# Performance work log

Measured on AMD Instinct MI355X. Metric: run time of the kernel, lower is better.

The kernel has to match this reference:

```python
import jax, jax.numpy as jnp
import numpy as np

DIN = 1024
DOUT = 1024

def setup_inputs() -> dict:
    key = jax.random.key(0)
    kx, kq, kk, kv = jax.random.split(key, 4)
    x = jax.random.normal(kx, (4, 2048, DIN), dtype=jnp.float32)
    s = 1.0 / np.sqrt(DIN)
    Wq = jax.random.uniform(kq, (DIN, DOUT), dtype=jnp.float32, minval=-s, maxval=s)
    Wk = jax.random.uniform(kk, (DIN, DOUT), dtype=jnp.float32, minval=-s, maxval=s)
    Wv = jax.random.uniform(kv, (DIN, DOUT), dtype=jnp.float32, minval=-s, maxval=s)
    return {"x": x, "Wq": Wq, "Wk": Wk, "Wv": Wv}

def reference(x, Wq, Wk, Wv):
    # q,k,v: [B, T, D]
    q = jnp.einsum('btd,de->bte', x, Wq)
    k = jnp.einsum('btd,de->bte', x, Wk)
    v = jnp.einsum('btd,de->bte', x, Wv)
    # scores: [B, T_q, T_k]; NOTE: no 1/sqrt(d) scaling in original
    scores = jnp.einsum('bqd,bkd->bqk', q, k)
    # Original applies softmax over dim=1 (the QUERY axis), faithfully kept
    weights = jax.nn.softmax(scores, axis=1)
    return jnp.einsum('bqk,bkd->bqd', weights, v)
```

## Files before the change

kernel.cpp:

```cpp
#include <hip/hip_runtime.h>

#define B_   4
#define T_   2048
#define D_   1024
#define MTOK 8192

typedef __attribute__((ext_vector_type(8))) _Float16 half8;
typedef __attribute__((ext_vector_type(4))) float    f32x4;

#define GLD(G, L) __builtin_amdgcn_global_load_lds(                       \
    (const __attribute__((address_space(1))) void*)(G),                   \
    (__attribute__((address_space(3))) void*)(L), 16, 0, 0)

#define BAR()   __builtin_amdgcn_s_barrier()
#define BARM()  asm volatile("s_barrier" ::: "memory")
#define LGKM0() do { asm volatile("s_waitcnt lgkmcnt(0)" ::: "memory");   \
                     __builtin_amdgcn_sched_barrier(0); } while (0)
#define VMW3()  asm volatile("s_waitcnt vmcnt(3)" ::: "memory")
#define VMW1()  asm volatile("s_waitcnt vmcnt(1)" ::: "memory")
#define VMW0()  asm volatile("s_waitcnt vmcnt(0)" ::: "memory")

__device__ __forceinline__ unsigned short f2h(float f) {
  return __builtin_bit_cast(unsigned short, (_Float16)f);
}
__device__ __forceinline__ float h2f(unsigned short u) {
  return (float)__builtin_bit_cast(_Float16, u);
}

__global__ __launch_bounds__(256) void tofp16_kernel(
    const float4* __restrict__ in, ushort4* __restrict__ out, int n4,
    float4* __restrict__ cs, int c4) {
  int i = blockIdx.x * 256 + threadIdx.x;
  if (i < c4) cs[i] = (float4){0.f, 0.f, 0.f, 0.f};
  if (i >= n4) return;
  float4 v = in[i];
  ushort4 h;
  h.x = f2h(v.x); h.y = f2h(v.y); h.z = f2h(v.z); h.w = f2h(v.w);
  out[i] = h;
}

__global__ __launch_bounds__(256) void wcat_t_kernel(
    const float* __restrict__ Wq, const float* __restrict__ Wk,
    const float* __restrict__ Wv, unsigned short* __restrict__ Wt) {
  __shared__ float tile[32][33];
  int z = blockIdx.z;
  const float* W = (z == 0) ? Wq : ((z == 1) ? Wk : Wv);
  int c0 = blockIdx.x * 32, r0 = blockIdx.y * 32;
  int tx = threadIdx.x & 31, ty = threadIdx.x >> 5;
  #pragma unroll
  for (int i = 0; i < 4; ++i)
    tile[ty + i * 8][tx] = W[(size_t)(r0 + ty + i * 8) * D_ + c0 + tx];
  __syncthreads();
  #pragma unroll
  for (int i = 0; i < 4; ++i) {
    float v = tile[tx][ty + i * 8];
    size_t row = (size_t)z * D_ + c0 + ty + i * 8;
    Wt[row * D_ + r0 + tx] = f2h(v);
  }
}

__global__ __launch_bounds__(256) void vtrans_kernel(
    const unsigned short* __restrict__ QKV, unsigned short* __restrict__ Vt) {
  __shared__ unsigned short tile[64][68];
  int b = blockIdx.z;
  int t0 = blockIdx.x * 64, d0 = blockIdx.y * 64;
  int l16 = threadIdx.x & 15, rr = threadIdx.x >> 4;
  const unsigned short* src =
      QKV + ((size_t)b * 2048 + t0 + rr) * 3072 + 2048 + d0 + l16 * 4;
  #pragma unroll
  for (int i = 0; i < 4; ++i) {
    ushort4 v = *(const ushort4*)(src + (size_t)i * 16 * 3072);
    *(ushort4*)&tile[rr + i * 16][l16 * 4] = v;
  }
  __syncthreads();
  unsigned short* dst = Vt + ((size_t)b * D_ + d0) * 2048 + t0;
  #pragma unroll
  for (int j = 0; j < 4; ++j) {
    int dd = rr + j * 16;
    int tt = l16 * 4;
    ushort4 v;
    v.x = tile[tt + 0][dd]; v.y = tile[tt + 1][dd];
    v.z = tile[tt + 2][dd]; v.w = tile[tt + 3][dd];
    *(ushort4*)(dst + (size_t)dd * 2048 + tt) = v;
  }
}

template <int EPI>
__global__ __launch_bounds__(512, 4) void gemm8p(
    const unsigned short* __restrict__ A, const unsigned short* __restrict__ B,
    void* __restrict__ C0, float* __restrict__ CS,
    int K, int lda, int ldb, int ldc,
    long aBatch, long bBatch, long cBatch) {
  constexpr int ABY  = 128 * 64;
  constexpr int BUFB = ABY + 16384;
  __shared__ __align__(16) char lds[2 * BUFB];

  const int z = blockIdx.z;
  A += (size_t)z * aBatch;
  B += (size_t)z * bBatch;

  const int nwg = gridDim.x * gridDim.y;
  int s = blockIdx.y * gridDim.x + blockIdx.x;
  s = (s & 7) * (nwg >> 3) + (s >> 3);
  const int bx = s % gridDim.x, by = s / gridDim.x;
  const int brow = by * 128, bcol = bx * 256;

  const int tid = threadIdx.x;
  const int wid = tid >> 6, lane = tid & 63;
  const int wr = wid >> 2, wc = wid & 3;
  const int l15 = lane & 15, g4 = lane >> 4;

  const int scol = ((lane & 3) ^ ((lane >> 3) & 3)) * 8;
  const int srow = lane >> 2;
  int aoff, adst, boffs[2], bdst[2];
  {
    int r0 = wid * 16;
    aoff = (brow + r0 + srow) * lda + scol;
    adst = r0 * 64;
    #pragma unroll
    for (int rg = 0; rg < 2; ++rg) {
      int rb = (wid >> 1) * 64 + rg * 32 + (wid & 1) * 16;
      boffs[rg] = (bcol + rb + srow) * ldb + scol;
      bdst[rg]  = ABY + rb * 64;
    }
  }

  const int rslot = (g4 ^ ((l15 >> 1) & 3)) * 16;
  int aRd[2], bRd[2];
  #pragma unroll
  for (int mh = 0; mh < 2; ++mh) {
    aRd[mh] = (wr * 64 + mh * 32 + l15) * 64 + rslot;
    bRd[mh] = ABY + (wc * 64 + mh * 32 + l15) * 64 + rslot;
  }

#define STAGE_A(bb, tt) \
    GLD(A + (size_t)(aoff + (tt) * 32), lds + (bb) * BUFB + adst)
#define STAGE_B(nh, bb, tt) \
    GLD(B + (size_t)(boffs[nh] + (tt) * 32), lds + (bb) * BUFB + bdst[nh])
#define LOAD_A(mh) do { _Pragma("unroll")                                     \
    for (int mf = 0; mf < 2; ++mf)                                            \
      ar[mf] = *(const half8*)(buf + aRd[mh] + mf * 1024); } while (0)
#define LOAD_B(dst, nh) do { _Pragma("unroll")                                \
    for (int nf = 0; nf < 2; ++nf)                                            \
      dst[nf] = *(const half8*)(buf + bRd[nh] + nf * 1024); } while (0)
#define MFMA_Q(mh, nh, br) do { _Pragma("unroll")                             \
    for (int mf = 0; mf < 2; ++mf) { _Pragma("unroll")                        \
      for (int nf = 0; nf < 2; ++nf) {                                        \
        f32x4& ac = acc[(mh) * 2 + mf][(nh) * 2 + nf];                        \
        ac = __builtin_amdgcn_mfma_f32_16x16x32_f16(ar[mf], br[nf], ac, 0, 0, 0); \
      } } } while (0)

  STAGE_A(0, 0); STAGE_B(0, 0, 0); STAGE_B(1, 0, 0);
  STAGE_A(1, 1); STAGE_B(0, 1, 1); STAGE_B(1, 1, 1);
  VMW3();
  BAR();

  f32x4 acc[4][4] = {};
  half8 ar[2], b0r[2], b1r[2];
  const int nIter = K / 64;

  for (int it = 0; it < nIter; ++it) {
    const bool st = (it + 1 < nIter);
    #pragma unroll
    for (int h = 0; h < 2; ++h) {
      const char* buf = lds + h * BUFB;
      const int tt = 2 * it + 2 + h;
      LOAD_A(0); LOAD_B(b0r, 0);
      BAR(); LGKM0();
      __builtin_amdgcn_s_setprio(1); MFMA_Q(0, 0, b0r);
      __builtin_amdgcn_s_setprio(0); BAR();
      LOAD_B(b1r, 1);
      if (st) STAGE_B(0, h, tt);
      BAR(); LGKM0();
      __builtin_amdgcn_s_setprio(1); MFMA_Q(0, 1, b1r);
      __builtin_amdgcn_s_setprio(0); BAR();
      LOAD_A(1);
      if (st) STAGE_B(1, h, tt);
      BAR(); LGKM0();
      __builtin_amdgcn_s_setprio(1); MFMA_Q(1, 1, b1r);
      __builtin_amdgcn_s_setprio(0); BAR();
      if (st) STAGE_A(h, tt);
      BAR();
      __builtin_amdgcn_s_setprio(1); MFMA_Q(1, 0, b0r);
      __builtin_amdgcn_s_setprio(0);
      if (st) { VMW3(); } else { VMW0(); }
      BAR();
    }
  }

  if constexpr (EPI == 1) {
    unsigned short* C = (unsigned short*)C0 + (size_t)z * cBatch;
    #pragma unroll
    for (int m = 0; m < 4; ++m) {
      int rowoff = (m >> 1) * 32 + (m & 1) * 16;
      #pragma unroll
      for (int n = 0; n < 4; ++n) {
        int coloff = (n >> 1) * 32 + (n & 1) * 16;
        #pragma unroll
        for (int r = 0; r < 4; ++r) {
          int row = brow + wr * 64 + rowoff + g4 * 4 + r;
          int col = bcol + wc * 64 + coloff + l15;
          C[(size_t)row * ldc + col] = f2h(acc[m][n][r]);
        }
      }
    }
  } else {
    unsigned short* C = (unsigned short*)C0 + (size_t)z * cBatch;
    float csum[4] = {0.f, 0.f, 0.f, 0.f};
    #pragma unroll
    for (int m = 0; m < 4; ++m) {
      int rowoff = (m >> 1) * 32 + (m & 1) * 16;
      #pragma unroll
      for (int n = 0; n < 4; ++n) {
        int coloff = (n >> 1) * 32 + (n & 1) * 16;
        #pragma unroll
        for (int r = 0; r < 4; ++r) {
          int row = brow + wr * 64 + rowoff + g4 * 4 + r;
          int col = bcol + wc * 64 + coloff + l15;
          unsigned short hh = f2h(acc[m][n][r]);
          C[(size_t)row * ldc + col] = hh;
          csum[n] += __expf(h2f(hh) - 64.0f);
        }
      }
    }
    #pragma unroll
    for (int n = 0; n < 4; ++n) {
      csum[n] += __shfl_xor(csum[n], 16);
      csum[n] += __shfl_xor(csum[n], 32);
    }
    if (g4 == 0) {
      #pragma unroll
      for (int n = 0; n < 4; ++n) {
        int col = bcol + wc * 64 + (n >> 1) * 32 + (n & 1) * 16 + l15;
        unsafeAtomicAdd(CS + (size_t)z * T_ + col, csum[n]);
      }
    }
  }
#undef STAGE_A
#undef STAGE_B
#undef LOAD_A
#undef LOAD_B
#undef MFMA_Q
}

__global__ __launch_bounds__(512, 4) void gemmPV(
    const unsigned short* __restrict__ Sc, const float* __restrict__ U,
    const unsigned short* __restrict__ Bv, float* __restrict__ out) {
  constexpr int ABY  = 128 * 64;
  constexpr int BUFB = ABY + 8192;
  __shared__ __align__(16) char lds[3 * BUFB];

  const int b = blockIdx.z;
  Sc += (size_t)b * T_ * T_;
  U  += (size_t)b * T_;
  Bv += (size_t)b * D_ * T_;
  float* Co = out + (size_t)b * T_ * D_;

  const int nwg = gridDim.x * gridDim.y;
  int s = blockIdx.y * gridDim.x + blockIdx.x;
  s = (s & 7) * (nwg >> 3) + (s >> 3);
  const int bx = s % gridDim.x, by = s / gridDim.x;
  const int brow = by * 128, bcol = bx * 128;

  const int tid = threadIdx.x;
  const int wid = tid >> 6, lane = tid & 63;
  const int wr = wid >> 2, wc = wid & 3;
  const int l15 = lane & 15, g4 = lane >> 4;

  const int arow = wid * 16 + (lane >> 2);
  const unsigned short* aSrc = Sc + (size_t)(brow + arow) * T_ + (lane & 3) * 8;
  const int awB  = arow * 64 + ((lane & 3) ^ ((lane >> 3) & 3)) * 16;
  const int ucol = (lane & 3) * 8;

  const int scol = ((lane & 3) ^ ((lane >> 3) & 3)) * 8;
  const int boff = (bcol + wid * 16 + (lane >> 2)) * T_ + scol;
  const int bdst = ABY + wid * 1024;

  const int rslot = (g4 ^ ((l15 >> 1) & 3)) * 16;
  int aRd[4], bRd[2];
  #pragma unroll
  for (int mf = 0; mf < 4; ++mf)
    aRd[mf] = (wr * 64 + mf * 16 + l15) * 64 + rslot;
  #pragma unroll
  for (int nf = 0; nf < 2; ++nf)
    bRd[nf] = ABY + (wc * 32 + nf * 16 + l15) * 64 + rslot;

  uint4 rawA;
  float4 uva, uvb;

#define PV_AISSUE(tt) do {                                                    \
    rawA = *(const uint4*)(aSrc + (size_t)(tt) * 32);                         \
    uva  = *(const float4*)(U + (tt) * 32 + ucol);                            \
    uvb  = *(const float4*)(U + (tt) * 32 + ucol + 4); } while (0)
#define PV_AWRITE(base) do {                                                  \
    const unsigned short* hp = (const unsigned short*)&rawA;                  \
    float uu[8] = {uva.x, uva.y, uva.z, uva.w, uvb.x, uvb.y, uvb.z, uvb.w};   \
    unsigned int w_[4];                                                       \
    _Pragma("unroll") for (int j = 0; j < 4; ++j) {                           \
      float w0 = __expf(h2f(hp[2 * j])     - 64.f) * uu[2 * j];               \
      float w1 = __expf(h2f(hp[2 * j + 1]) - 64.f) * uu[2 * j + 1];           \
      w_[j] = (unsigned int)f2h(w0) | ((unsigned int)f2h(w1) << 16); }        \
    *(uint4*)((base) + awB) = *(uint4*)w_; } while (0)

  char* bufA = lds;
  char* bufB = lds + BUFB;
  char* bufC = lds + 2 * BUFB;

  PV_AISSUE(0);
  GLD(Bv + (size_t)(boff + 0), bufA + bdst);
  uint4  rawA1 = *(const uint4*)(aSrc + 32);
  float4 uva1  = *(const float4*)(U + 32 + ucol);
  float4 uvb1  = *(const float4*)(U + 32 + ucol + 4);
  GLD(Bv + (size_t)(boff + 32), bufB + bdst);
  VMW1();
  PV_AWRITE(bufA);
  rawA = rawA1; uva = uva1; uvb = uvb1;
  PV_AWRITE(bufB);
  asm volatile("s_waitcnt lgkmcnt(0)" ::: "memory");

  f32x4 acc[4][2] = {};
  half8 ar[4], br[2];
  const int NT = T_ / 32;

  for (int t = 0; t < NT; ++t) {
    BARM();
    const bool st = (t + 2 < NT);
    if (st) {
      PV_AISSUE(t + 2);
      GLD(Bv + (size_t)(boff + (t + 2) * 32), bufC + bdst);
    }
    #pragma unroll
    for (int mf = 0; mf < 4; ++mf)
      ar[mf] = *(const half8*)(bufA + aRd[mf]);
    #pragma unroll
    for (int nf = 0; nf < 2; ++nf)
      br[nf] = *(const half8*)(bufA + bRd[nf]);
    __builtin_amdgcn_s_setprio(1);
    #pragma unroll
    for (int mf = 0; mf < 4; ++mf)
      #pragma unroll
      for (int nf = 0; nf < 2; ++nf)
        acc[mf][nf] = __builtin_amdgcn_mfma_f32_16x16x32_f16(ar[mf], br[nf], acc[mf][nf], 0, 0, 0);
    __builtin_amdgcn_s_setprio(0);
    if (st) {
      VMW1();
      PV_AWRITE(bufC);
      asm volatile("s_waitcnt lgkmcnt(0)" ::: "memory");
    } else if (t + 2 == NT) {
      VMW0();
    }
    char* tmp = bufA; bufA = bufB; bufB = bufC; bufC = tmp;
  }

  #pragma unroll
  for (int mf = 0; mf < 4; ++mf)
    #pragma unroll
    for (int nf = 0; nf < 2; ++nf)
      #pragma unroll
      for (int r = 0; r < 4; ++r) {
        int row = brow + wr * 64 + mf * 16 + g4 * 4 + r;
        int col = bcol + wc * 32 + nf * 16 + l15;
        Co[(size_t)row * D_ + col] = acc[mf][nf][r];
      }
#undef PV_AISSUE
#undef PV_AWRITE
}

__global__ __launch_bounds__(256) void sm_stats(const float* __restrict__ cs,
                                                float* __restrict__ stats) {
  int i = blockIdx.x * 256 + threadIdx.x;
  stats[i] = 1.0f / cs[i];
}

extern "C" void kernel_launch(void* const* d_in, const int* in_sizes, int n_in,
                              void* d_out, int out_size, void* d_ws, size_t ws_size,
                              hipStream_t stream) {
  const float* x  = (const float*)d_in[0];
  const float* Wq = (const float*)d_in[1];
  const float* Wk = (const float*)d_in[2];
  const float* Wv = (const float*)d_in[3];
  float* out = (float*)d_out;

  char* ws = (char*)d_ws;
  const size_t MB = 1024ull * 1024ull;
  unsigned short* scoresh = (unsigned short*)(ws);
  unsigned short* QKVh = (unsigned short*)(ws + 32 * MB);
  unsigned short* Vt   = (unsigned short*)(ws + 80 * MB);
  unsigned short* xh   = (unsigned short*)(ws + 96 * MB);
  unsigned short* Wt   = (unsigned short*)(ws + 112 * MB);
  float* colsum = (float*)(ws + 118 * MB);
  float* stats  = (float*)(ws + 118 * MB + 64 * 1024);

  tofp16_kernel<<<MTOK * D_ / 4 / 256, 256, 0, stream>>>(
      (const float4*)x, (ushort4*)xh, MTOK * D_ / 4,
      (float4*)colsum, B_ * T_ / 4);

  wcat_t_kernel<<<dim3(32, 32, 3), 256, 0, stream>>>(Wq, Wk, Wv, Wt);

  gemm8p<1><<<dim3(3072 / 256, MTOK / 128, 1), 512, 0, stream>>>(
      xh, Wt, QKVh, nullptr, D_, D_, D_, 3072, 0, 0, 0);

  vtrans_kernel<<<dim3(T_ / 64, D_ / 64, B_), 256, 0, stream>>>(QKVh, Vt);

  gemm8p<2><<<dim3(T_ / 256, T_ / 128, B_), 512, 0, stream>>>(
      QKVh, QKVh + 1024, scoresh, colsum, D_, 3072, 3072, T_,
      (long)T_ * 3072, (long)T_ * 3072, (long)T_ * T_);

  sm_stats<<<B_ * T_ / 256, 256, 0, stream>>>(colsum, stats);

  gemmPV<<<dim3(D_ / 128, T_ / 128, B_), 512, 0, stream>>>(
      scoresh, stats, Vt, out);
}
```

Before: 201.5 us.

## Retile PV GEMM to 64x256 blocks with 4 waves, 64x64 per wave

Reshapes the PV GEMM tile from 128x128 with 8 waves to 64x256 with 4 waves, so each wave computes a 64x64 output block. Each wave reuses A fragments across more B columns, and the exp/scale transform of scores is done for only 64 rows per block, which cuts redundant exp work per output element. The cost is higher register pressure from doubling the accumulators, fewer waves per block, a larger B staging buffer, and changed vmcnt wait counts.

```diff
diff --git a/kernel.cpp b/kernel.cpp
--- a/kernel.cpp
+++ b/kernel.cpp
@@ -16,9 +16,7 @@
 #define BARM()  asm volatile("s_barrier" ::: "memory")
 #define LGKM0() do { asm volatile("s_waitcnt lgkmcnt(0)" ::: "memory");   \
                      __builtin_amdgcn_sched_barrier(0); } while (0)
-#define VMW3()  asm volatile("s_waitcnt vmcnt(3)" ::: "memory")
-#define VMW1()  asm volatile("s_waitcnt vmcnt(1)" ::: "memory")
-#define VMW0()  asm volatile("s_waitcnt vmcnt(0)" ::: "memory")
+#define VMW(n)  asm volatile("s_waitcnt vmcnt(" #n ")" ::: "memory")
 
 __device__ __forceinline__ unsigned short f2h(float f) {
   return __builtin_bit_cast(unsigned short, (_Float16)f);
@@ -152,7 +150,7 @@
 
   STAGE_A(0, 0); STAGE_B(0, 0, 0); STAGE_B(1, 0, 0);
   STAGE_A(1, 1); STAGE_B(0, 1, 1); STAGE_B(1, 1, 1);
-  VMW3();
+  VMW(3);
   BAR();
 
   f32x4 acc[4][4] = {};
@@ -183,7 +181,7 @@
       BAR();
       __builtin_amdgcn_s_setprio(1); MFMA_Q(1, 0, b0r);
       __builtin_amdgcn_s_setprio(0);
-      if (st) { VMW3(); } else { VMW0(); }
+      if (st) { VMW(3); } else { VMW(0); }
       BAR();
     }
   }
@@ -243,11 +241,11 @@
 #undef MFMA_Q
 }
 
-__global__ __launch_bounds__(512, 4) void gemmPV(
+__global__ __launch_bounds__(256, 2) void gemmPV(
     const unsigned short* __restrict__ Sc, const float* __restrict__ U,
     const unsigned short* __restrict__ Bv, float* __restrict__ out) {
-  constexpr int ABY  = 128 * 64;
-  constexpr int BUFB = ABY + 8192;
+  constexpr int ABY  = 64 * 64;
+  constexpr int BUFB = ABY + 16384;
   __shared__ __align__(16) char lds[3 * BUFB];
 
   const int b = blockIdx.z;
@@ -260,34 +258,42 @@
   int s = blockIdx.y * gridDim.x + blockIdx.x;
   s = (s & 7) * (nwg >> 3) + (s >> 3);
   const int bx = s % gridDim.x, by = s / gridDim.x;
-  const int brow = by * 128, bcol = bx * 128;
+  const int brow = by * 64, bcol = bx * 256;
 
   const int tid = threadIdx.x;
   const int wid = tid >> 6, lane = tid & 63;
-  const int wr = wid >> 2, wc = wid & 3;
   const int l15 = lane & 15, g4 = lane >> 4;
 
-  const int arow = wid * 16 + (lane >> 2);
-  const unsigned short* aSrc = Sc + (size_t)(brow + arow) * T_ + (lane & 3) * 8;
-  const int awB  = arow * 64 + ((lane & 3) ^ ((lane >> 3) & 3)) * 16;
-  const int ucol = (lane & 3) * 8;
+  const int arow = tid >> 2;
+  const unsigned short* aSrc = Sc + (size_t)(brow + arow) * T_ + (tid & 3) * 8;
+  const int awB  = arow * 64 + ((tid & 3) ^ ((tid >> 3) & 3)) * 16;
+  const int ucol = (tid & 3) * 8;
 
   const int scol = ((lane & 3) ^ ((lane >> 3) & 3)) * 8;
-  const int boff = (bcol + wid * 16 + (lane >> 2)) * T_ + scol;
-  const int bdst = ABY + wid * 1024;
+  const int srow = lane >> 2;
+  int boffs[4], bdst[4];
+  #pragma unroll
+  for (int g = 0; g < 4; ++g) {
+    int rb = g * 64 + wid * 16;
+    boffs[g] = (bcol + rb + srow) * T_ + scol;
+    bdst[g]  = ABY + rb * 64;
+  }
 
   const int rslot = (g4 ^ ((l15 >> 1) & 3)) * 16;
-  int aRd[4], bRd[2];
+  int aRd[4], bRd[4];
   #pragma unroll
   for (int mf = 0; mf < 4; ++mf)
-    aRd[mf] = (wr * 64 + mf * 16 + l15) * 64 + rslot;
-  #pragma unroll
-  for (int nf = 0; nf < 2; ++nf)
-    bRd[nf] = ABY + (wc * 32 + nf * 16 + l15) * 64 + rslot;
+    aRd[mf] = (mf * 16 + l15) * 64 + rslot;
+  #pragma unroll
+  for (int nf = 0; nf < 4; ++nf)
+    bRd[nf] = ABY + (wid * 64 + nf * 16 + l15) * 64 + rslot;
 
   uint4 rawA;
   float4 uva, uvb;
 
+#define PV_BSTAGE(base, tt) do { _Pragma("unroll")                            \
+    for (int g = 0; g < 4; ++g)                                               \
+      GLD(Bv + (size_t)(boffs[g] + (tt) * 32), (base) + bdst[g]); } while (0)
 #define PV_AISSUE(tt) do {                                                    \
     rawA = *(const uint4*)(aSrc + (size_t)(tt) * 32);                         \
     uva  = *(const float4*)(U + (tt) * 32 + ucol);                            \
@@ -307,19 +313,20 @@
   char* bufC = lds + 2 * BUFB;
 
   PV_AISSUE(0);
-  GLD(Bv + (size_t)(boff + 0), bufA + bdst);
+  PV_BSTAGE(bufA, 0);
   uint4  rawA1 = *(const uint4*)(aSrc + 32);
   float4 uva1  = *(const float4*)(U + 32 + ucol);
   float4 uvb1  = *(const float4*)(U + 32 + ucol + 4);
-  GLD(Bv + (size_t)(boff + 32), bufB + bdst);
-  VMW1();
+  PV_BSTAGE(bufB, 1);
+  VMW(11);
   PV_AWRITE(bufA);
+  VMW(4);
   rawA = rawA1; uva = uva1; uvb = uvb1;
   PV_AWRITE(bufB);
   asm volatile("s_waitcnt lgkmcnt(0)" ::: "memory");
 
-  f32x4 acc[4][2] = {};
-  half8 ar[4], br[2];
+  f32x4 acc[4][4] = {};
+  half8 ar[4], br[4];
   const int NT = T_ / 32;
 
   for (int t = 0; t < NT; ++t) {
@@ -327,27 +334,27 @@
     const bool st = (t + 2 < NT);
     if (st) {
       PV_AISSUE(t + 2);
-      GLD(Bv + (size_t)(boff + (t + 2) * 32), bufC + bdst);
+      PV_BSTAGE(bufC, t + 2);
     }
     #pragma unroll
     for (int mf = 0; mf < 4; ++mf)
       ar[mf] = *(const half8*)(bufA + aRd[mf]);
     #pragma unroll
-    for (int nf = 0; nf < 2; ++nf)
+    for (int nf = 0; nf < 4; ++nf)
       br[nf] = *(const half8*)(bufA + bRd[nf]);
     __builtin_amdgcn_s_setprio(1);
     #pragma unroll
     for (int mf = 0; mf < 4; ++mf)
       #pragma unroll
-      for (int nf = 0; nf < 2; ++nf)
+      for (int nf = 0; nf < 4; ++nf)
         acc[mf][nf] = __builtin_amdgcn_mfma_f32_16x16x32_f16(ar[mf], br[nf], acc[mf][nf], 0, 0, 0);
     __builtin_amdgcn_s_setprio(0);
     if (st) {
-      VMW1();
+      VMW(4);
       PV_AWRITE(bufC);
       asm volatile("s_waitcnt lgkmcnt(0)" ::: "memory");
     } else if (t + 2 == NT) {
-      VMW0();
+      VMW(0);
     }
     char* tmp = bufA; bufA = bufB; bufB = bufC; bufC = tmp;
   }
@@ -355,13 +362,14 @@
   #pragma unroll
   for (int mf = 0; mf < 4; ++mf)
     #pragma unroll
-    for (int nf = 0; nf < 2; ++nf)
+    for (int nf = 0; nf < 4; ++nf)
       #pragma unroll
       for (int r = 0; r < 4; ++r) {
-        int row = brow + wr * 64 + mf * 16 + g4 * 4 + r;
-        int col = bcol + wc * 32 + nf * 16 + l15;
+        int row = brow + mf * 16 + g4 * 4 + r;
+        int col = bcol + wid * 64 + nf * 16 + l15;
         Co[(size_t)row * D_ + col] = acc[mf][nf][r];
       }
+#undef PV_BSTAGE
 #undef PV_AISSUE
 #undef PV_AWRITE
 }
@@ -408,6 +416,6 @@
 
   sm_stats<<<B_ * T_ / 256, 256, 0, stream>>>(colsum, stats);
 
-  gemmPV<<<dim3(D_ / 128, T_ / 128, B_), 512, 0, stream>>>(
+  gemmPV<<<dim3(D_ / 256, T_ / 64, B_), 256, 0, stream>>>(
       scoresh, stats, Vt, out);
 }
```

Result: no change. 198.3 us (median of 2 runs) (-1.6%).
